# Performance work log

Hardware: AMD Instinct MI355X
Metric: run time of the kernel (lower is better)

## Reference

```python
import jax, jax.numpy as jnp
import numpy as np

N_HEAD = 16
D_HEAD = 64
N_GROUPS = 4
D_EMBED = 1024
ROPE_N = 32
B, T = 2, 2048


def apply_rope(x, cos, sin):
    # x: (..., T, ROPE_N); cos/sin: (T, ROPE_N) broadcast over leading dims
    h = x.shape[-1]
    x1, x2 = x[..., : h // 2], x[..., h // 2 :]
    rotated = jnp.concatenate((-x2, x1), axis=-1)
    return (x * cos + rotated * sin).astype(x.dtype)


def setup_inputs() -> dict:
    key = jax.random.key(0)
    k1, k2, k3, k4, k5 = jax.random.split(key, 5)
    return {
        "x": jax.random.normal(k1, (B, T, D_EMBED), dtype=jnp.float32),
        "cos": jax.random.uniform(k2, (T, ROPE_N), dtype=jnp.float32),
        "sin": jax.random.uniform(k3, (T, ROPE_N), dtype=jnp.float32),
        "mask": jnp.ones((B, T), dtype=bool),  # unused by the original forward (passes None to SDPA)
        "Wqkv": jax.random.normal(k4, (D_EMBED, (N_HEAD + 2 * N_GROUPS) * D_HEAD), dtype=jnp.float32) * 0.02,
        "Wout": jax.random.normal(k5, (N_HEAD * D_HEAD, D_EMBED), dtype=jnp.float32) * 0.02,
    }


def reference(x, cos, sin, mask, Wqkv, Wout):
    Bv, Tv, _ = x.shape
    q_per_kv = N_HEAD // N_GROUPS  # 4
    total_qkv = q_per_kv + 2       # 6

    qkv = jnp.einsum("btc,cf->btf", x, Wqkv)  # (B, T, 1536)
    qkv = qkv.reshape(Bv, Tv, N_GROUPS, total_qkv, D_HEAD)
    qkv = jnp.transpose(qkv, (0, 2, 3, 1, 4))  # (B, G, total_qkv, T, d)

    q = qkv[:, :, :q_per_kv]           # (B, G, q_per_kv, T, d)
    k = qkv[:, :, q_per_kv : q_per_kv + 1]  # (B, G, 1, T, d)
    v = qkv[:, :, q_per_kv + 1 :]           # (B, G, 1, T, d)

    # GQA expand (1 < groups < heads)
    k = jnp.broadcast_to(k, (Bv, N_GROUPS, q_per_kv, Tv, D_HEAD))
    v = jnp.broadcast_to(v, (Bv, N_GROUPS, q_per_kv, Tv, D_HEAD))

    q = q.reshape(Bv, N_HEAD, Tv, D_HEAD)
    k = k.reshape(Bv, N_HEAD, Tv, D_HEAD)
    v = v.reshape(Bv, N_HEAD, Tv, D_HEAD)

    # partial RoPE on the first ROPE_N dims of each head
    q = jnp.concatenate((apply_rope(q[..., :ROPE_N], cos, sin), q[..., ROPE_N:]), axis=-1)
    k = jnp.concatenate((apply_rope(k[..., :ROPE_N], cos, sin), k[..., ROPE_N:]), axis=-1)

    scale = 1.0 / np.sqrt(D_HEAD).astype(np.float32)
    scores = jnp.einsum("bhtd,bhsd->bhts", q, k) * scale
    attn = jax.nn.softmax(scores, axis=-1)
    y = jnp.einsum("bhts,bhsd->bhtd", attn, v)   # (B, H, T, d)
    y = jnp.transpose(y, (0, 2, 1, 3)).reshape(Bv, Tv, N_HEAD * D_HEAD)
    return jnp.einsum("btf,fc->btc", y, Wout)
```

## Files before the change

### kernel.cpp

```cpp
#include <hip/hip_runtime.h>
#include <hip/hip_bf16.h>
#include <math.h>

#define BATCH   2
#define TSEQ    2048
#define DEMBED  1024
#define NHEAD   16
#define DHEAD   64
#define NGROUP  4
#define ROPEN   32
#define FQKV    1536
#define MROWS   (BATCH*TSEQ)

typedef __attribute__((ext_vector_type(8))) short short8;
typedef __attribute__((ext_vector_type(4))) float floatx4;

__device__ __forceinline__ void split_pack8(const float* f, uint4& h4, uint4& l4) {
    uint u[8], lu[8];
    #pragma unroll
    for (int j = 0; j < 8; ++j) {
        u[j] = __float_as_uint(f[j]);
        float lf = f[j] - __uint_as_float(u[j] & 0xffff0000u);
        lu[j] = __float_as_uint(lf);
    }
    h4.x = __builtin_amdgcn_perm(u[1], u[0], 0x07060302u);
    h4.y = __builtin_amdgcn_perm(u[3], u[2], 0x07060302u);
    h4.z = __builtin_amdgcn_perm(u[5], u[4], 0x07060302u);
    h4.w = __builtin_amdgcn_perm(u[7], u[6], 0x07060302u);
    l4.x = __builtin_amdgcn_perm(lu[1], lu[0], 0x07060302u);
    l4.y = __builtin_amdgcn_perm(lu[3], lu[2], 0x07060302u);
    l4.z = __builtin_amdgcn_perm(lu[5], lu[4], 0x07060302u);
    l4.w = __builtin_amdgcn_perm(lu[7], lu[6], 0x07060302u);
}

__device__ __forceinline__ void rtn_pack8(const float* f, uint4& h4) {
    uint t[8];
    #pragma unroll
    for (int j = 0; j < 8; ++j)
        t[j] = __float_as_uint(f[j]) + 0x8000u;
    h4.x = __builtin_amdgcn_perm(t[1], t[0], 0x07060302u);
    h4.y = __builtin_amdgcn_perm(t[3], t[2], 0x07060302u);
    h4.z = __builtin_amdgcn_perm(t[5], t[4], 0x07060302u);
    h4.w = __builtin_amdgcn_perm(t[7], t[6], 0x07060302u);
}

__device__ __forceinline__ ushort bf16_rtn(float x) {
    return (ushort)((__float_as_uint(x) + 0x8000u) >> 16);
}

__device__ __forceinline__ void lds_async16(void* lds, const void* gp) {
    __builtin_amdgcn_global_load_lds(
        (const __attribute__((address_space(1))) unsigned int*)gp,
        (__attribute__((address_space(3))) unsigned int*)lds,
        16, 0, 0);
}


__global__ __launch_bounds__(256) void conv_xy(const float* __restrict__ in,
                                               char* __restrict__ img) {
    const int tid = threadIdx.x;
    const int c   = blockIdx.x & 15;
    const int mt  = blockIdx.x >> 4;
    const int r    = tid >> 1;
    const int half = tid & 1;

    const float* src = in + (size_t)(mt*128 + r)*1024 + c*64 + half*32;
    float f[32];
    #pragma unroll
    for (int u = 0; u < 8; ++u)
        *(float4*)(f + 4*u) = *(const float4*)(src + 4*u);

    char* tile = img + ((size_t)(mt*16 + c)) * 32768;
    #pragma unroll
    for (int cc = 0; cc < 4; ++cc) {
        uint4 h4, l4;
        split_pack8(f + cc*8, h4, l4);
        int j    = half*4 + cc;
        int phys = j ^ (r & 7);
        *(uint4*)(tile + r*128 + phys*16)         = h4;
        *(uint4*)(tile + 16384 + r*128 + phys*16) = l4;
    }
}

__global__ __launch_bounds__(256) void conv_w(const float* __restrict__ W,
                                              int N,
                                              char* __restrict__ img) {
    __shared__ float Lf[64][132];
    const int tid = threadIdx.x;
    const int c   = blockIdx.x;
    const int nt  = blockIdx.y;

    {
        const int kk = tid >> 2;
        const int nc = (tid & 3) * 32;
        const float* src = W + (size_t)(c*64 + kk)*N + nt*128 + nc;
        #pragma unroll
        for (int u = 0; u < 8; ++u)
            *(float4*)(&Lf[kk][nc + 4*u]) = *(const float4*)(src + 4*u);
    }
    __syncthreads();

    char* tile = img + ((size_t)(nt*16 + c)) * 32768;
    #pragma unroll
    for (int rep = 0; rep < 4; ++rep) {
        int idx = rep*256 + tid;
        int n = idx & 127;
        int j = idx >> 7;
        float v[8];
        #pragma unroll
        for (int i = 0; i < 8; ++i) v[i] = Lf[j*8 + i][n];
        uint4 h4, l4;
        split_pack8(v, h4, l4);
        int phys = j ^ (n & 7);
        *(uint4*)(tile + n*128 + phys*16)         = h4;
        *(uint4*)(tile + 16384 + n*128 + phys*16) = l4;
    }
}

struct GemmAcc { floatx4 a[4][4]; };

__device__ __forceinline__ void gemm_mfma_core(const char* __restrict__ Aimg,
                                               const char* __restrict__ Bimg,
                                               char* smem, int mt, int nt,
                                               int tid, GemmAcc& G) {
    const int wv = tid >> 6;
    const int wm = wv & 1, wn = wv >> 1;
    const int lane = tid & 63;
    const int qd = lane >> 4, cl = lane & 15;
    const int wslot = (tid & 192) * 16;

    #pragma unroll
    for (int tm = 0; tm < 4; ++tm)
        #pragma unroll
        for (int tn = 0; tn < 4; ++tn)
            G.a[tm][tn] = (floatx4){0.f, 0.f, 0.f, 0.f};

    for (int c = 0; c < 16; ++c) {
        __syncthreads();
        {
            const uint4* gA = (const uint4*)(Aimg + ((size_t)(mt*16 + c)) * 32768) + tid;
            const uint4* gB = (const uint4*)(Bimg + ((size_t)(nt*16 + c)) * 32768) + tid;
            #pragma unroll
            for (int j = 0; j < 8; ++j) {
                lds_async16(smem + j*4096 + wslot,         gA + j*256);
                lds_async16(smem + 32768 + j*4096 + wslot, gB + j*256);
            }
        }
        __syncthreads();

        #pragma unroll
        for (int s = 0; s < 2; ++s) {
            const int phys = ((s*4 + qd) ^ (cl & 7)) * 16;
            short8 ah[4], al[4], bh[4], bl[4];
            #pragma unroll
            for (int tt = 0; tt < 4; ++tt) {
                const int rA = wm*64 + 16*tt + cl;
                ah[tt] = *(const short8*)(smem + rA*128 + phys);
                al[tt] = *(const short8*)(smem + 16384 + rA*128 + phys);
                const int rB = wn*64 + 16*tt + cl;
                bh[tt] = *(const short8*)(smem + 32768 + rB*128 + phys);
                bl[tt] = *(const short8*)(smem + 49152 + rB*128 + phys);
            }
            #pragma unroll
            for (int tm = 0; tm < 4; ++tm)
                #pragma unroll
                for (int tn = 0; tn < 4; ++tn) {
                    G.a[tm][tn] = __builtin_amdgcn_mfma_f32_16x16x32_bf16(ah[tm], bh[tn], G.a[tm][tn], 0, 0, 0);
                    G.a[tm][tn] = __builtin_amdgcn_mfma_f32_16x16x32_bf16(al[tm], bh[tn], G.a[tm][tn], 0, 0, 0);
                    G.a[tm][tn] = __builtin_amdgcn_mfma_f32_16x16x32_bf16(ah[tm], bl[tn], G.a[tm][tn], 0, 0, 0);
                }
        }
    }
}

__global__ __launch_bounds__(256, 2) void gemm_qkv_mfma(const char* __restrict__ Aimg,
                                                        const char* __restrict__ Bimg,
                                                        const float* __restrict__ cosp,
                                                        const float* __restrict__ sinp,
                                                        float* __restrict__ Qf,
                                                        ushort* __restrict__ Kimg,
                                                        ushort* __restrict__ Vimg) {
    __shared__ __align__(16) char smem[68608];
    const int tid = threadIdx.x;
    const int nt = blockIdx.x, mt = blockIdx.y;

    GemmAcc G;
    gemm_mfma_core(Aimg, Bimg, smem, mt, nt, tid, G);

    const int wv = tid >> 6;
    const int wm = wv & 1, wn = wv >> 1;
    const int lane = tid & 63;
    const int qd = lane >> 4, cl = lane & 15;

    const int slice = nt*2 + wn;
    const int g  = slice / 6;
    const int jj = slice % 6;
    const int b  = mt >> 4;

    if (jj != 5) {
        #pragma unroll
        for (int tm = 0; tm < 4; ++tm)
            #pragma unroll
            for (int r = 0; r < 4; ++r) {
                int m = mt*128 + wm*64 + 16*tm + 4*qd + r;
                int t = m & 2047;
                float c1 = cosp[t*ROPEN + cl],      s1 = sinp[t*ROPEN + cl];
                float c2 = cosp[t*ROPEN + 16 + cl], s2 = sinp[t*ROPEN + 16 + cl];
                float x1 = G.a[tm][0][r], x2 = G.a[tm][1][r];
                G.a[tm][0][r] = x1*c1 - x2*s1;
                G.a[tm][1][r] = x2*c2 + x1*s2;
            }
    }

    if (jj < 4) {
        #pragma unroll
        for (int tm = 0; tm < 4; ++tm)
            #pragma unroll
            for (int tn = 0; tn < 4; ++tn)
                #pragma unroll
                for (int r = 0; r < 4; ++r) {
                    int m = mt*128 + wm*64 + 16*tm + 4*qd + r;
                    Qf[(size_t)m*1024 + (g*4 + jj)*64 + 16*tn + cl] = G.a[tm][tn][r];
                }
    } else {
        float* Lw = (float*)(smem + wv*17152);
        __syncthreads();
        #pragma unroll
        for (int tm = 0; tm < 4; ++tm)
            #pragma unroll
            for (int tn = 0; tn < 4; ++tn)
                #pragma unroll
                for (int r = 0; r < 4; ++r)
                    Lw[(16*tm + 4*qd + r)*67 + 16*tn + cl] = G.a[tm][tn][r];
        __syncthreads();

        const int cloc = (mt & 15)*2 + wm;
        ushort* img = ((jj == 4) ? Kimg : Vimg)
                      + (size_t)(b*4 + g)*262144 + (size_t)cloc*8192;
        if (jj == 4) {
            const int rr = lane;
            float f[8];
            #pragma unroll
            for (int ch = 0; ch < 8; ++ch) {
                *(float4*)f       = *(const float4*)(&Lw[rr*67 + ch*8]);
                *(float4*)(f + 4) = *(const float4*)(&Lw[rr*67 + ch*8 + 4]);
                uint4 h4, l4;
                split_pack8(f, h4, l4);
                int phys = ch ^ (rr & 7);
                *(uint4*)(img + rr*64 + phys*8)        = h4;
                *(uint4*)(img + 4096 + rr*64 + phys*8) = l4;
            }
        } else {
            const int d = lane;
            float f[8];
            #pragma unroll
            for (int ch = 0; ch < 8; ++ch) {
                #pragma unroll
                for (int i = 0; i < 8; ++i) f[i] = Lw[(ch*8 + i)*67 + d];
                uint4 h4;
                rtn_pack8(f, h4);
                int phys = ch ^ (d & 7);
                *(uint4*)(img + d*64 + phys*8) = h4;
            }
        }
    }
}

__global__ __launch_bounds__(256, 2) void gemm_out_mfma(const char* __restrict__ Aimg,
                                                        const char* __restrict__ Bimg,
                                                        float* __restrict__ C) {
    __shared__ __align__(16) char smem[49152];
    const int tid = threadIdx.x;
    const int nt = blockIdx.x, mt = blockIdx.y;

    const int wv = tid >> 6;
    const int wm = wv & 1, wn = wv >> 1;
    const int lane = tid & 63;
    const int qd = lane >> 4, cl = lane & 15;
    const int wslot = (tid & 192) * 16;

    floatx4 acc[2][4];
    #pragma unroll
    for (int tm = 0; tm < 2; ++tm)
        #pragma unroll
        for (int tn = 0; tn < 4; ++tn)
            acc[tm][tn] = (floatx4){0.f, 0.f, 0.f, 0.f};

    for (int c = 0; c < 16; ++c) {
        __syncthreads();
        {
            const char* sA = Aimg + ((size_t)((mt >> 1)*16 + c))*32768
                                  + (mt & 1)*8192 + (size_t)tid*16;
            const char* sB = Bimg + ((size_t)(nt*16 + c))*32768 + (size_t)tid*16;
            lds_async16(smem + wslot,          sA);
            lds_async16(smem + 4096  + wslot,  sA + 4096);
            lds_async16(smem + 8192  + wslot,  sA + 16384);
            lds_async16(smem + 12288 + wslot,  sA + 16384 + 4096);
            #pragma unroll
            for (int j = 0; j < 4; ++j) {
                lds_async16(smem + 16384 + j*4096 + wslot, sB + j*4096);
                lds_async16(smem + 32768 + j*4096 + wslot, sB + 16384 + j*4096);
            }
        }
        __syncthreads();

        #pragma unroll
        for (int s = 0; s < 2; ++s) {
            const int phys = ((s*4 + qd) ^ (cl & 7)) * 16;
            short8 ah[2], al[2], bh[4], bl[4];
            #pragma unroll
            for (int tt = 0; tt < 2; ++tt) {
                const int rA = wm*32 + 16*tt + cl;
                ah[tt] = *(const short8*)(smem + rA*128 + phys);
                al[tt] = *(const short8*)(smem + 8192 + rA*128 + phys);
            }
            #pragma unroll
            for (int tt = 0; tt < 4; ++tt) {
                const int rB = wn*64 + 16*tt + cl;
                bh[tt] = *(const short8*)(smem + 16384 + rB*128 + phys);
                bl[tt] = *(const short8*)(smem + 32768 + rB*128 + phys);
            }
            #pragma unroll
            for (int tm = 0; tm < 2; ++tm)
                #pragma unroll
                for (int tn = 0; tn < 4; ++tn) {
                    acc[tm][tn] = __builtin_amdgcn_mfma_f32_16x16x32_bf16(ah[tm], bh[tn], acc[tm][tn], 0, 0, 0);
                    acc[tm][tn] = __builtin_amdgcn_mfma_f32_16x16x32_bf16(al[tm], bh[tn], acc[tm][tn], 0, 0, 0);
                    acc[tm][tn] = __builtin_amdgcn_mfma_f32_16x16x32_bf16(ah[tm], bl[tn], acc[tm][tn], 0, 0, 0);
                }
        }
    }

    #pragma unroll
    for (int tm = 0; tm < 2; ++tm)
        #pragma unroll
        for (int tn = 0; tn < 4; ++tn)
            #pragma unroll
            for (int r = 0; r < 4; ++r) {
                int m = mt*64 + wm*32 + 16*tm + 4*qd + r;
                int n = nt*128 + wn*64 + 16*tn + cl;
                C[(size_t)m*1024 + n] = acc[tm][tn][r];
            }
}

__global__ __launch_bounds__(256, 4) void attn8(const float* __restrict__ Qf,
                                                const char* __restrict__ Kimg,
                                                const char* __restrict__ Vimg,
                                                char* __restrict__ Yimg) {
    __shared__ __align__(16) char smem[20992];
    ushort* Pp = (ushort*)(smem + 16384);

    const int tid  = threadIdx.x;
    const int wv   = tid >> 6;
    const int lane = tid & 63;
    const int qd   = lane >> 4;
    const int cl   = lane & 15;

    const int bg    = blockIdx.x & 7;
    const int inner = blockIdx.x >> 3;
    const int hj    = inner >> 5;
    const int qt    = inner & 31;
    const int b = bg >> 2, g = bg & 3;
    const int h = g*4 + hj;

    short8 qh[2], ql[2];
    {
        const float* qp = Qf + (size_t)(b*2048 + qt*64 + wv*16 + cl)*1024
                             + h*64 + 8*qd;
        #pragma unroll
        for (int s = 0; s < 2; ++s) {
            float f[8];
            *(float4*)f       = *(const float4*)(qp + 32*s);
            *(float4*)(f + 4) = *(const float4*)(qp + 32*s + 4);
            #pragma unroll
            for (int i = 0; i < 8; ++i) f[i] *= 0.125f;
            uint4 h4, l4;
            split_pack8(f, h4, l4);
            qh[s] = __builtin_bit_cast(short8, h4);
            ql[s] = __builtin_bit_cast(short8, l4);
        }
    }

    floatx4 accO[4] = {};
    float lsum[4] = {};

    const char* Kg0 = Kimg + (size_t)bg*524288;
    const char* Vg0 = Vimg + (size_t)bg*524288;
    const int wslot = (tid & 192) * 16;

    {
        const char* src = Kg0 + (size_t)tid*16;
        lds_async16(smem + wslot,        src);
        lds_async16(smem + 4096 + wslot, src + 8192);
    }

    for (int c = 0; c < TSEQ/32; ++c) {
        __syncthreads();
        const int buf = c & 1;
        if (c + 1 < TSEQ/32) {
            const int nb = (c + 1) & 1;
            const char* src = Kg0 + (size_t)((c+1) >> 1)*16384
                                  + ((c+1) & 1)*4096 + (size_t)tid*16;
            lds_async16(smem + nb*8192 + wslot,        src);
            lds_async16(smem + nb*8192 + 4096 + wslot, src + 8192);
        }
        const char* Kl = smem + buf*8192;

        floatx4 accS[2] = {};
        __builtin_amdgcn_s_setprio(1);
        #pragma unroll
        for (int s = 0; s < 2; ++s) {
            #pragma unroll
            for (int tt = 0; tt < 2; ++tt) {
                const int off = (16*tt + cl)*128 + (((4*s + qd) ^ (cl & 7))*16);
                short8 bh = *(const short8*)(Kl + off);
                short8 bl = *(const short8*)(Kl + 4096 + off);
                accS[tt] = __builtin_amdgcn_mfma_f32_16x16x32_bf16(qh[s], bh, accS[tt], 0, 0, 0);
                accS[tt] = __builtin_amdgcn_mfma_f32_16x16x32_bf16(ql[s], bh, accS[tt], 0, 0, 0);
                accS[tt] = __builtin_amdgcn_mfma_f32_16x16x32_bf16(qh[s], bl, accS[tt], 0, 0, 0);
            }
        }
        __builtin_amdgcn_s_setprio(0);

        #pragma unroll
        for (int r = 0; r < 4; ++r) {
            float p0 = __expf(accS[0][r]);
            float p1 = __expf(accS[1][r]);
            lsum[r] += p0 + p1;
            ushort* prow = Pp + (16*wv + 4*qd + r)*36 + cl;
            prow[0]  = bf16_rtn(p0);
            prow[16] = bf16_rtn(p1);
        }

        const char* Vg = Vg0 + (size_t)(c >> 1)*16384;
        short8 pa = *(const short8*)(Pp + (16*wv + cl)*36 + 8*qd);
        __builtin_amdgcn_s_setprio(1);
        #pragma unroll
        for (int tt = 0; tt < 4; ++tt) {
            const int off = (16*tt + cl)*128 + ((((c & 1)*4 + qd) ^ (cl & 7))*16);
            short8 vh = *(const short8*)(Vg + off);
            accO[tt] = __builtin_amdgcn_mfma_f32_16x16x32_bf16(pa, vh, accO[tt], 0, 0, 0);
        }
        __builtin_amdgcn_s_setprio(0);
    }

    __syncthreads();
    float* Lt = (float*)smem;
    #pragma unroll
    for (int r = 0; r < 4; ++r) {
        float l = lsum[r];
        l += __shfl_xor(l, 1);
        l += __shfl_xor(l, 2);
        l += __shfl_xor(l, 4);
        l += __shfl_xor(l, 8);
        float inv = 1.0f / l;
        int row = 16*wv + 4*qd + r;
        Lt[row*66 + cl]      = accO[0][r] * inv;
        Lt[row*66 + 16 + cl] = accO[1][r] * inv;
        Lt[row*66 + 32 + cl] = accO[2][r] * inv;
        Lt[row*66 + 48 + cl] = accO[3][r] * inv;
    }
    __syncthreads();
    {
        const int r0 = tid >> 2;
        const int qq = tid & 3;
        float f[16];
        #pragma unroll
        for (int u = 0; u < 8; ++u)
            *(float2*)(f + 2*u) = *(const float2*)(&Lt[r0*66 + qq*16 + 2*u]);
        const int R = (qt & 1)*64 + r0;
        char* tile = Yimg + (size_t)((b*16 + (qt >> 1))*16 + h) * 32768;
        #pragma unroll
        for (int cc = 0; cc < 2; ++cc) {
            uint4 h4, l4;
            split_pack8(f + 8*cc, h4, l4);
            int j    = qq*2 + cc;
            int phys = j ^ (R & 7);
            *(uint4*)(tile + R*128 + phys*16)         = h4;
            *(uint4*)(tile + 16384 + R*128 + phys*16) = l4;
        }
    }
}

extern "C" void kernel_launch(void* const* d_in, const int* in_sizes, int n_in,
                              void* d_out, int out_size, void* d_ws, size_t ws_size,
                              hipStream_t stream) {
    const float* x    = (const float*)d_in[0];
    const float* cosp = (const float*)d_in[1];
    const float* sinp = (const float*)d_in[2];
    const float* Wqkv = (const float*)d_in[4];
    const float* Wout = (const float*)d_in[5];
    float* out = (float*)d_out;

    char* ws = (char*)d_ws;
    float*  Qf    = (float*)(ws);
    ushort* Kimg  = (ushort*)(ws + ((size_t)16<<20));
    ushort* Vimg  = (ushort*)(ws + ((size_t)20<<20));
    char*   Bo    = ws + ((size_t)24<<20);
    char*   Ximg  = ws + ((size_t)28<<20);
    char*   Bq    = ws + ((size_t)44<<20);
    char*   Yimg  = ws + ((size_t)28<<20);

    conv_xy<<<512, 256, 0, stream>>>(x, Ximg);
    conv_w<<<dim3(16, 12), 256, 0, stream>>>(Wqkv, FQKV, Bq);
    conv_w<<<dim3(16, 8), 256, 0, stream>>>(Wout, DEMBED, Bo);
    gemm_qkv_mfma<<<dim3(12, 32), 256, 0, stream>>>(Ximg, Bq, cosp, sinp,
                                                    Qf, Kimg, Vimg);
    attn8<<<1024, 256, 0, stream>>>(Qf, (const char*)Kimg, (const char*)Vimg,
                                    Yimg);
    gemm_out_mfma<<<dim3(8, 64), 256, 0, stream>>>(Yimg, Bo, out);
}
```

Before: 252.5 us.

## Transpose attention MFMAs, process 64-key chunks, use exp2 with packed P stores

The attention kernel now computes S^T and O^T by swapping the MFMA operands, so each lane owns one query row. This makes the P tile writable as packed bf16 pairs and reduces the row-sum to two shuffles. The key loop now advances 64 keys per barrier with a 16KB double-buffered K tile, which halves the number of __syncthreads. The log2(e) factor is folded into the Q scale so raw v_exp_f32 can replace __expf. LDS use grows to about 37KB per block, which may limit occupancy.

```diff
diff --git a/kernel.cpp b/kernel.cpp
--- a/kernel.cpp
+++ b/kernel.cpp
@@ -44,8 +44,16 @@
     h4.w = __builtin_amdgcn_perm(t[7], t[6], 0x07060302u);
 }
 
-__device__ __forceinline__ ushort bf16_rtn(float x) {
-    return (ushort)((__float_as_uint(x) + 0x8000u) >> 16);
+__device__ __forceinline__ uint pk_bf16x2(float f0, float f1) {
+    uint u0 = __float_as_uint(f0) + 0x8000u;
+    uint u1 = __float_as_uint(f1) + 0x8000u;
+    return __builtin_amdgcn_perm(u1, u0, 0x07060302u);
+}
+
+__device__ __forceinline__ float fast_exp2(float x) {
+    float r;
+    asm("v_exp_f32 %0, %1" : "=v"(r) : "v"(x));
+    return r;
 }
 
 __device__ __forceinline__ void lds_async16(void* lds, const void* gp) {
@@ -343,12 +351,12 @@
             }
 }
 
-__global__ __launch_bounds__(256, 4) void attn8(const float* __restrict__ Qf,
-                                                const char* __restrict__ Kimg,
-                                                const char* __restrict__ Vimg,
-                                                char* __restrict__ Yimg) {
-    __shared__ __align__(16) char smem[20992];
-    ushort* Pp = (ushort*)(smem + 16384);
+__global__ __launch_bounds__(256, 4) void attn10(const float* __restrict__ Qf,
+                                                 const char* __restrict__ Kimg,
+                                                 const char* __restrict__ Vimg,
+                                                 char* __restrict__ Yimg) {
+    __shared__ __align__(16) char smem[37888];
+    uint* Pp32 = (uint*)(smem + 32768);
 
     const int tid  = threadIdx.x;
     const int wv   = tid >> 6;
@@ -373,7 +381,7 @@
             *(float4*)f       = *(const float4*)(qp + 32*s);
             *(float4*)(f + 4) = *(const float4*)(qp + 32*s + 4);
             #pragma unroll
-            for (int i = 0; i < 8; ++i) f[i] *= 0.125f;
+            for (int i = 0; i < 8; ++i) f[i] *= 0.125f * 1.44269504088896f;
             uint4 h4, l4;
             split_pack8(f, h4, l4);
             qh[s] = __builtin_bit_cast(short8, h4);
@@ -381,8 +389,8 @@
         }
     }
 
-    floatx4 accO[4] = {};
-    float lsum[4] = {};
+    floatx4 accOT[4] = {};
+    float lsum = 0.f;
 
     const char* Kg0 = Kimg + (size_t)bg*524288;
     const char* Vg0 = Vimg + (size_t)bg*524288;
@@ -390,75 +398,84 @@
 
     {
         const char* src = Kg0 + (size_t)tid*16;
-        lds_async16(smem + wslot,        src);
-        lds_async16(smem + 4096 + wslot, src + 8192);
-    }
-
-    for (int c = 0; c < TSEQ/32; ++c) {
+        #pragma unroll
+        for (int j = 0; j < 4; ++j)
+            lds_async16(smem + j*4096 + wslot, src + j*4096);
+    }
+
+    for (int c = 0; c < TSEQ/64; ++c) {
         __syncthreads();
         const int buf = c & 1;
-        if (c + 1 < TSEQ/32) {
-            const int nb = (c + 1) & 1;
-            const char* src = Kg0 + (size_t)((c+1) >> 1)*16384
-                                  + ((c+1) & 1)*4096 + (size_t)tid*16;
-            lds_async16(smem + nb*8192 + wslot,        src);
-            lds_async16(smem + nb*8192 + 4096 + wslot, src + 8192);
-        }
-        const char* Kl = smem + buf*8192;
-
-        floatx4 accS[2] = {};
-        __builtin_amdgcn_s_setprio(1);
-        #pragma unroll
-        for (int s = 0; s < 2; ++s) {
-            #pragma unroll
-            for (int tt = 0; tt < 2; ++tt) {
-                const int off = (16*tt + cl)*128 + (((4*s + qd) ^ (cl & 7))*16);
-                short8 bh = *(const short8*)(Kl + off);
-                short8 bl = *(const short8*)(Kl + 4096 + off);
-                accS[tt] = __builtin_amdgcn_mfma_f32_16x16x32_bf16(qh[s], bh, accS[tt], 0, 0, 0);
-                accS[tt] = __builtin_amdgcn_mfma_f32_16x16x32_bf16(ql[s], bh, accS[tt], 0, 0, 0);
-                accS[tt] = __builtin_amdgcn_mfma_f32_16x16x32_bf16(qh[s], bl, accS[tt], 0, 0, 0);
-            }
-        }
-        __builtin_amdgcn_s_setprio(0);
-
-        #pragma unroll
-        for (int r = 0; r < 4; ++r) {
-            float p0 = __expf(accS[0][r]);
-            float p1 = __expf(accS[1][r]);
-            lsum[r] += p0 + p1;
-            ushort* prow = Pp + (16*wv + 4*qd + r)*36 + cl;
-            prow[0]  = bf16_rtn(p0);
-            prow[16] = bf16_rtn(p1);
-        }
-
-        const char* Vg = Vg0 + (size_t)(c >> 1)*16384;
-        short8 pa = *(const short8*)(Pp + (16*wv + cl)*36 + 8*qd);
-        __builtin_amdgcn_s_setprio(1);
-        #pragma unroll
-        for (int tt = 0; tt < 4; ++tt) {
-            const int off = (16*tt + cl)*128 + ((((c & 1)*4 + qd) ^ (cl & 7))*16);
-            short8 vh = *(const short8*)(Vg + off);
-            accO[tt] = __builtin_amdgcn_mfma_f32_16x16x32_bf16(pa, vh, accO[tt], 0, 0, 0);
-        }
-        __builtin_amdgcn_s_setprio(0);
+        if (c + 1 < TSEQ/64) {
+            const char* src = Kg0 + (size_t)(c+1)*16384 + (size_t)tid*16;
+            #pragma unroll
+            for (int j = 0; j < 4; ++j)
+                lds_async16(smem + (1-buf)*16384 + j*4096 + wslot, src + j*4096);
+        }
+        const char* Kl = smem + buf*16384;
+        const char* Vg = Vg0 + (size_t)c*16384;
+
+        #pragma unroll
+        for (int hh = 0; hh < 2; ++hh) {
+            floatx4 accST[2] = {};
+            __builtin_amdgcn_s_setprio(1);
+            #pragma unroll
+            for (int s = 0; s < 2; ++s) {
+                #pragma unroll
+                for (int tt = 0; tt < 2; ++tt) {
+                    const int off = (32*hh + 16*tt + cl)*128
+                                  + (((4*s + qd) ^ (cl & 7))*16);
+                    short8 kh = *(const short8*)(Kl + off);
+                    short8 kl = *(const short8*)(Kl + 8192 + off);
+                    accST[tt] = __builtin_amdgcn_mfma_f32_16x16x32_bf16(kh, qh[s], accST[tt], 0, 0, 0);
+                    accST[tt] = __builtin_amdgcn_mfma_f32_16x16x32_bf16(kh, ql[s], accST[tt], 0, 0, 0);
+                    accST[tt] = __builtin_amdgcn_mfma_f32_16x16x32_bf16(kl, qh[s], accST[tt], 0, 0, 0);
+                }
+            }
+            __builtin_amdgcn_s_setprio(0);
+
+            float p[8];
+            #pragma unroll
+            for (int tt = 0; tt < 2; ++tt)
+                #pragma unroll
+                for (int r = 0; r < 4; ++r)
+                    p[4*tt + r] = fast_exp2(accST[tt][r]);
+            lsum += ((p[0] + p[1]) + (p[2] + p[3]))
+                  + ((p[4] + p[5]) + (p[6] + p[7]));
+            {
+                uint* prow = Pp32 + (16*wv + cl)*20 + 2*qd;
+                uint2 w0; w0.x = pk_bf16x2(p[0], p[1]); w0.y = pk_bf16x2(p[2], p[3]);
+                uint2 w1; w1.x = pk_bf16x2(p[4], p[5]); w1.y = pk_bf16x2(p[6], p[7]);
+                *(uint2*)(prow)     = w0;
+                *(uint2*)(prow + 8) = w1;
+            }
+
+            uint4 paw = *(const uint4*)(Pp32 + (16*wv + cl)*20 + 4*qd);
+            short8 pa = __builtin_bit_cast(short8, paw);
+            __builtin_amdgcn_s_setprio(1);
+            #pragma unroll
+            for (int tt = 0; tt < 4; ++tt) {
+                const int off = (16*tt + cl)*128 + (((4*hh + qd) ^ (cl & 7))*16);
+                short8 vh = *(const short8*)(Vg + off);
+                accOT[tt] = __builtin_amdgcn_mfma_f32_16x16x32_bf16(vh, pa, accOT[tt], 0, 0, 0);
+            }
+            __builtin_amdgcn_s_setprio(0);
+        }
     }
 
     __syncthreads();
     float* Lt = (float*)smem;
-    #pragma unroll
-    for (int r = 0; r < 4; ++r) {
-        float l = lsum[r];
-        l += __shfl_xor(l, 1);
-        l += __shfl_xor(l, 2);
-        l += __shfl_xor(l, 4);
-        l += __shfl_xor(l, 8);
+    {
+        float l = lsum;
+        l += __shfl_xor(l, 16);
+        l += __shfl_xor(l, 32);
         float inv = 1.0f / l;
-        int row = 16*wv + 4*qd + r;
-        Lt[row*66 + cl]      = accO[0][r] * inv;
-        Lt[row*66 + 16 + cl] = accO[1][r] * inv;
-        Lt[row*66 + 32 + cl] = accO[2][r] * inv;
-        Lt[row*66 + 48 + cl] = accO[3][r] * inv;
+        const int row = 16*wv + cl;
+        #pragma unroll
+        for (int tt = 0; tt < 4; ++tt)
+            #pragma unroll
+            for (int r = 0; r < 4; ++r)
+                Lt[row*66 + 16*tt + 4*qd + r] = accOT[tt][r] * inv;
     }
     __syncthreads();
     {
@@ -506,7 +523,7 @@
     conv_w<<<dim3(16, 8), 256, 0, stream>>>(Wout, DEMBED, Bo);
     gemm_qkv_mfma<<<dim3(12, 32), 256, 0, stream>>>(Ximg, Bq, cosp, sinp,
                                                     Qf, Kimg, Vimg);
-    attn8<<<1024, 256, 0, stream>>>(Qf, (const char*)Kimg, (const char*)Vimg,
-                                    Yimg);
+    attn10<<<1024, 256, 0, stream>>>(Qf, (const char*)Kimg, (const char*)Vimg,
+                                     Yimg);
     gemm_out_mfma<<<dim3(8, 64), 256, 0, stream>>>(Yimg, Bo, out);
 }
```

Measured after the change: 241.0 us. 1.05x faster.
